# Kernel optimization log

Hardware: AMD Instinct MI355X
Metric: run time of the kernel (lower is better)

The kernel has to match this reference:

```python
import jax, jax.numpy as jnp
import numpy as np

HIDDEN = 2048
NUM_HEADS = 16
HEAD_DIM = HIDDEN // NUM_HEADS


def setup_inputs() -> dict:
    key = jax.random.key(0)
    k1, k2, k3 = jax.random.split(key, 3)
    hidden_states = jax.random.normal(k1, (4, 2048, HIDDEN), dtype=jnp.float32)
    # torch Linear weight is (out, in); y = x @ W.T. Store transposed (in, out).
    w_qkv = jax.random.normal(k2, (HIDDEN, 3 * HIDDEN), dtype=jnp.float32) * (HIDDEN ** -0.5)
    w_o = jax.random.normal(k3, (HIDDEN, HIDDEN), dtype=jnp.float32) * (HIDDEN ** -0.5)
    return {"hidden_states": hidden_states, "w_qkv": w_qkv, "w_o": w_o}


def reference(hidden_states, w_qkv, w_o):
    B, S, _ = hidden_states.shape
    qkv = hidden_states @ w_qkv  # (B, S, 3*HIDDEN)
    # Faithful to torch .view: row-major reshape straight to (B, H, S, 3*head_dim)
    qkv = qkv.reshape(B, NUM_HEADS, S, 3 * HEAD_DIM)
    q, k, v = jnp.split(qkv, 3, axis=-1)  # each (B, H, S, head_dim)
    scores = jnp.einsum('bhsd,bhtd->bhst', q, k) / (HEAD_DIM ** 0.5)
    probs = jax.nn.softmax(scores, axis=-1)
    attn = jnp.einsum('bhst,bhtd->bhsd', probs, v)  # (B, H, S, head_dim)
    # Faithful to torch .reshape(B, S, hidden) without transpose
    attn = attn.reshape(B, S, HIDDEN)
    return attn @ w_o
```

## Files before the change

### kernel.cpp

```cpp
#include <hip/hip_runtime.h>
#include <stdint.h>

#define DEVINL __device__ __forceinline__

typedef __attribute__((ext_vector_type(8))) __bf16 bf16x8;
typedef __attribute__((ext_vector_type(4))) float f32x4;
typedef __attribute__((ext_vector_type(16))) float f32x16;

static constexpr int HID  = 2048;
static constexpr int NQ   = 6144;
static constexpr int SEQ  = 2048;
static constexpr int NB   = 4;
static constexpr int MTOT = NB * SEQ;

DEVINL unsigned short f2bf(float f) {
  union { float f; uint32_t u; } x; x.f = f;
  uint32_t r = x.u + 0x7fffu + ((x.u >> 16) & 1u);
  return (unsigned short)(r >> 16);
}

DEVINL float fexp2(float x) { float r; asm("v_exp_f32 %0, %1" : "=v"(r) : "v"(x)); return r; }

typedef const __attribute__((address_space(1))) void gvoid_t;
typedef __attribute__((address_space(3))) void svoid_t;

DEVINL void gload_lds16(const void* g, void* s) {
  __builtin_amdgcn_global_load_lds((gvoid_t*)(uintptr_t)g,
                                   (svoid_t*)(uint32_t)(uintptr_t)s,
                                   16, 0, 0);
}


__global__ void k_cvt(const float* __restrict__ in, unsigned short* __restrict__ out, int n4) {
  int i = blockIdx.x * blockDim.x + threadIdx.x;
  if (i >= n4) return;
  float4 v = ((const float4*)in)[i];
  ushort4 o;
  o.x = f2bf(v.x); o.y = f2bf(v.y); o.z = f2bf(v.z); o.w = f2bf(v.w);
  ((ushort4*)out)[i] = o;
}

__global__ void k_transpose_cvt(const float* __restrict__ in, unsigned short* __restrict__ out,
                                int R, int C) {
  __shared__ float tile[32][33];
  int c0 = blockIdx.x * 32, r0 = blockIdx.y * 32;
  int tx = threadIdx.x & 31, ty = threadIdx.x >> 5;
  #pragma unroll
  for (int i = 0; i < 32; i += 8)
    tile[ty + i][tx] = in[(size_t)(r0 + ty + i) * C + (c0 + tx)];
  __syncthreads();
  #pragma unroll
  for (int i = 0; i < 32; i += 8)
    out[(size_t)(c0 + ty + i) * R + (r0 + tx)] = f2bf(tile[tx][ty + i]);
}


template <int OUT_BF16, int QSCALE>
__global__ __launch_bounds__(256, 2) void k_gemm2(const unsigned short* __restrict__ A,
                                                  const unsigned short* __restrict__ BT,
                                                  void* __restrict__ Cout,
                                                  int M, int N, int K) {
  __shared__ unsigned short As[256 * 64];
  __shared__ unsigned short Bs[128 * 64];
  const int tid = threadIdx.x;
  const int w = tid >> 6, l = tid & 63;
  const int lane16 = l & 15, lgrp = l >> 4;
  const int bn = blockIdx.x, bm = blockIdx.y;
  const int srow = l >> 3;
  const int gslot = (l & 7) ^ (l >> 3);

  f32x4 acc[4][8] = {};

  for (int k0 = 0; k0 < K; k0 += 64) {
    #pragma unroll
    for (int i = 0; i < 8; ++i) {
      const int chunk = i * 4 + w;
      const int row = chunk * 8 + srow;
      gload_lds16(A + (size_t)(bm * 256 + row) * K + k0 + gslot * 8, As + chunk * 512);
    }
    #pragma unroll
    for (int i = 0; i < 4; ++i) {
      const int chunk = i * 4 + w;
      const int row = chunk * 8 + srow;
      gload_lds16(BT + (size_t)(bn * 128 + row) * K + k0 + gslot * 8, Bs + chunk * 512);
    }
    __syncthreads();

    #pragma unroll
    for (int kk = 0; kk < 2; ++kk) {
      bf16x8 af[4], bfr[8];
      #pragma unroll
      for (int mf = 0; mf < 4; ++mf) {
        const int row = w * 64 + mf * 16 + lane16;
        af[mf] = *(const bf16x8*)(As + row * 64 + (((kk * 4 + lgrp) ^ (row & 7)) * 8));
      }
      #pragma unroll
      for (int nf = 0; nf < 8; ++nf) {
        const int row = nf * 16 + lane16;
        bfr[nf] = *(const bf16x8*)(Bs + row * 64 + (((kk * 4 + lgrp) ^ (row & 7)) * 8));
      }
      #pragma unroll
      for (int mf = 0; mf < 4; ++mf)
        #pragma unroll
        for (int nf = 0; nf < 8; ++nf)
          acc[mf][nf] = __builtin_amdgcn_mfma_f32_16x16x32_bf16(af[mf], bfr[nf], acc[mf][nf], 0, 0, 0);
    }
    __syncthreads();
  }

  const float qs = (QSCALE && (bn % 3 == 0)) ? 0.12751744f : 1.0f;
  const size_t row0 = (size_t)bm * 256 + w * 64;
  const int col0 = bn * 128;
  #pragma unroll
  for (int mf = 0; mf < 4; ++mf) {
    #pragma unroll
    for (int nf = 0; nf < 8; ++nf) {
      const int col = col0 + nf * 16 + lane16;
      #pragma unroll
      for (int r = 0; r < 4; ++r) {
        const size_t row = row0 + mf * 16 + lgrp * 4 + r;
        if (OUT_BF16)
          ((unsigned short*)Cout)[row * N + col] = f2bf(acc[mf][nf][r] * qs);
        else
          ((float*)Cout)[row * N + col] = acc[mf][nf][r];
      }
    }
  }
}

__global__ __launch_bounds__(256, 2) void k_build_vt2(const unsigned short* __restrict__ QKV,
                                                      unsigned short* __restrict__ Vt) {
  __shared__ unsigned short lt[128][136];
  const int head = blockIdx.y;
  const int tblk = blockIdx.x;
  const int b = head >> 4, h = head & 15;
  const int base_row = b * SEQ + h * 128;
  const int tid = threadIdx.x;

  #pragma unroll
  for (int it = 0; it < 8; ++it) {
    const int idx = it * 256 + tid;
    const int tt = idx >> 4, dgrp = idx & 15;
    const uint4 v = *(const uint4*)(QKV + (size_t)(base_row + tblk * 8 + (tt >> 4)) * NQ
                                        + (tt & 15) * 384 + 256 + dgrp * 8);
    *(uint4*)(&lt[tt][dgrp * 8]) = v;
  }
  __syncthreads();

  #pragma unroll
  for (int it = 0; it < 8; ++it) {
    const int idx = it * 256 + tid;
    const int d = idx >> 4, tgrp = idx & 15;
    ushort4 a, bq;
    a.x = lt[tgrp * 8 + 0][d]; a.y = lt[tgrp * 8 + 1][d];
    a.z = lt[tgrp * 8 + 2][d]; a.w = lt[tgrp * 8 + 3][d];
    bq.x = lt[tgrp * 8 + 4][d]; bq.y = lt[tgrp * 8 + 5][d];
    bq.z = lt[tgrp * 8 + 6][d]; bq.w = lt[tgrp * 8 + 7][d];
    unsigned short* dst = Vt + ((size_t)head * 128 + d) * SEQ + tblk * 128 + tgrp * 8;
    *(ushort4*)(dst) = a;
    *(ushort4*)(dst + 4) = bq;
  }
}

__global__ __launch_bounds__(256, 2) void k_attn(const unsigned short* __restrict__ QKV,
                                                 const unsigned short* __restrict__ Vt,
                                                 unsigned short* __restrict__ ATT) {
  __shared__ unsigned short Ks[2][64 * 128];
  __shared__ unsigned short Vs[128 * 64];
  const int tid = threadIdx.x, w = tid >> 6, l = tid & 63;
  const int l32 = l & 31, hi = l >> 5;
  const int qt = blockIdx.x, head = blockIdx.y;
  const int b = head >> 4, h = head & 15;
  const float THR = 11.5415603f;
  const int base_row = b * SEQ + h * 128;

  const int s = qt * 128 + w * 32 + l32;
  bf16x8 qf[8];
  {
    const unsigned short* qrow = QKV + (size_t)(base_row + (s >> 4)) * NQ + (s & 15) * 384;
    #pragma unroll
    for (int dsl = 0; dsl < 8; ++dsl)
      qf[dsl] = *(const bf16x8*)(qrow + dsl * 16 + hi * 8);
  }

  f32x16 oacc[4] = {};
  float mrun = -1e30f, lrun = 0.0f;

  #define STAGE_K(bb, kv0)                                                               \
    {                                                                                    \
      _Pragma("unroll")                                                                  \
      for (int i = 0; i < 4; ++i) {                                                      \
        const int chunk = i * 4 + w;                                                     \
        const int r = chunk * 4 + (l >> 4);                                              \
        const int colsw = ((l & 15) ^ (r & 15)) * 8;                                     \
        gload_lds16(QKV + (size_t)(base_row + ((kv0) >> 4) + (r >> 4)) * NQ              \
                        + (r & 15) * 384 + 128 + colsw,                                  \
                    &Ks[bb][chunk * 512]);                                               \
      }                                                                                  \
    }
  #define STAGE_V(kv0)                                                                   \
    {                                                                                    \
      _Pragma("unroll")                                                                  \
      for (int i = 0; i < 4; ++i) {                                                      \
        const int chunk = i * 4 + w;                                                     \
        const int dr = chunk * 8 + (l >> 3);                                             \
        const int colsw = ((l & 7) ^ (dr & 7)) * 8;                                      \
        gload_lds16(Vt + ((size_t)head * 128 + dr) * SEQ + (kv0) + colsw,                \
                    &Vs[chunk * 512]);                                                   \
      }                                                                                  \
    }

  STAGE_K(0, 0);
  STAGE_V(0);
  __syncthreads();

  int kb = 0;
  for (int kv0 = 0; kv0 < SEQ; kv0 += 64) {
    const int next = kv0 + 64;
    if (next < SEQ) STAGE_K(kb ^ 1, next);

    f32x16 sacc[2] = {};
    __builtin_amdgcn_s_setprio(1);
    #pragma unroll
    for (int kvf = 0; kvf < 2; ++kvf) {
      const int row = kvf * 32 + l32;
      const unsigned short* kbase = &Ks[kb][row * 128];
      const int rs = (row & 15) << 3;
      #pragma unroll
      for (int dsl = 0; dsl < 8; ++dsl) {
        bf16x8 kf = *(const bf16x8*)(kbase + ((dsl * 16 + hi * 8) ^ rs));
        sacc[kvf] = __builtin_amdgcn_mfma_f32_32x32x16_bf16(kf, qf[dsl], sacc[kvf], 0, 0, 0);
      }
    }
    __builtin_amdgcn_s_setprio(0);

    float mx[16];
    #pragma unroll
    for (int r = 0; r < 16; ++r) mx[r] = fmaxf(sacc[0][r], sacc[1][r]);
    #pragma unroll
    for (int st = 8; st >= 1; st >>= 1)
      #pragma unroll
      for (int r = 0; r < st; ++r) mx[r] = fmaxf(mx[r], mx[r + st]);
    float pmax = fmaxf(mx[0], __shfl_xor(mx[0], 32));

    if (!__all(pmax - mrun <= THR)) {
      const float mnew = fmaxf(mrun, pmax);
      const float corr = fexp2(mrun - mnew);
      #pragma unroll
      for (int df = 0; df < 4; ++df)
        #pragma unroll
        for (int r = 0; r < 16; ++r) oacc[df][r] *= corr;
      lrun *= corr;
      mrun = mnew;
    }

    float ps[16];
    #pragma unroll
    for (int r = 0; r < 16; ++r) {
      const float p0 = fexp2(sacc[0][r] - mrun);
      const float p1 = fexp2(sacc[1][r] - mrun);
      sacc[0][r] = p0; sacc[1][r] = p1;
      ps[r] = p0 + p1;
    }
    #pragma unroll
    for (int st = 8; st >= 1; st >>= 1)
      #pragma unroll
      for (int r = 0; r < st; ++r) ps[r] += ps[r + st];
    lrun += ps[0] + __shfl_xor(ps[0], 32);

    bf16x8 pf[4];
    #pragma unroll
    for (int f = 0; f < 2; ++f) {
      unsigned int c0, c1, c2, c3, c4, c5, c6, c7;
      asm("v_cvt_pk_bf16_f32 %0, %1, %2" : "=v"(c0) : "v"(sacc[f][0]),  "v"(sacc[f][1]));
      asm("v_cvt_pk_bf16_f32 %0, %1, %2" : "=v"(c1) : "v"(sacc[f][2]),  "v"(sacc[f][3]));
      asm("v_cvt_pk_bf16_f32 %0, %1, %2" : "=v"(c2) : "v"(sacc[f][4]),  "v"(sacc[f][5]));
      asm("v_cvt_pk_bf16_f32 %0, %1, %2" : "=v"(c3) : "v"(sacc[f][6]),  "v"(sacc[f][7]));
      asm("v_cvt_pk_bf16_f32 %0, %1, %2" : "=v"(c4) : "v"(sacc[f][8]),  "v"(sacc[f][9]));
      asm("v_cvt_pk_bf16_f32 %0, %1, %2" : "=v"(c5) : "v"(sacc[f][10]), "v"(sacc[f][11]));
      asm("v_cvt_pk_bf16_f32 %0, %1, %2" : "=v"(c6) : "v"(sacc[f][12]), "v"(sacc[f][13]));
      asm("v_cvt_pk_bf16_f32 %0, %1, %2" : "=v"(c7) : "v"(sacc[f][14]), "v"(sacc[f][15]));
      asm("v_permlane32_swap_b32 %0, %1" : "+v"(c0), "+v"(c2));
      asm("v_permlane32_swap_b32 %0, %1" : "+v"(c1), "+v"(c3));
      asm("v_permlane32_swap_b32 %0, %1" : "+v"(c4), "+v"(c6));
      asm("v_permlane32_swap_b32 %0, %1" : "+v"(c5), "+v"(c7));
      union { unsigned int u[4]; bf16x8 v; } u0, u1;
      u0.u[0] = c0; u0.u[1] = c1; u0.u[2] = c2; u0.u[3] = c3;
      u1.u[0] = c4; u1.u[1] = c5; u1.u[2] = c6; u1.u[3] = c7;
      pf[2 * f] = u0.v; pf[2 * f + 1] = u1.v;
    }

    __syncthreads();

    __builtin_amdgcn_s_setprio(1);
    #pragma unroll
    for (int ks = 0; ks < 4; ++ks) {
      #pragma unroll
      for (int df = 0; df < 4; ++df) {
        const int row = df * 32 + l32;
        bf16x8 vf = *(const bf16x8*)(&Vs[row * 64 + (((ks * 16 + hi * 8) ^ ((row & 7) << 3)))]);
        oacc[df] = __builtin_amdgcn_mfma_f32_32x32x16_bf16(vf, pf[ks], oacc[df], 0, 0, 0);
      }
    }
    __builtin_amdgcn_s_setprio(0);

    __syncthreads();
    if (next < SEQ) STAGE_V(next);
    kb ^= 1;
  }

  const float inv = 1.0f / lrun;
  unsigned short* orow = ATT + (size_t)(base_row + (s >> 4)) * HID + (s & 15) * 128;
  #pragma unroll
  for (int df = 0; df < 4; ++df) {
    #pragma unroll
    for (int k = 0; k < 4; ++k) {
      ushort4 o;
      o.x = f2bf(oacc[df][4 * k + 0] * inv);
      o.y = f2bf(oacc[df][4 * k + 1] * inv);
      o.z = f2bf(oacc[df][4 * k + 2] * inv);
      o.w = f2bf(oacc[df][4 * k + 3] * inv);
      *(ushort4*)(orow + df * 32 + 8 * k + 4 * hi) = o;
    }
  }
}


extern "C" void kernel_launch(void* const* d_in, const int* in_sizes, int n_in,
                              void* d_out, int out_size, void* d_ws, size_t ws_size,
                              hipStream_t stream) {
  const float* X    = (const float*)d_in[0];
  const float* Wqkv = (const float*)d_in[1];
  const float* Wo   = (const float*)d_in[2];
  float* OUT = (float*)d_out;

  char* ws = (char*)d_ws;
  constexpr size_t SZ_QKV   = (size_t)MTOT * NQ * 2;
  constexpr size_t SZ_XBF   = (size_t)MTOT * HID * 2;
  constexpr size_t SZ_WQKVT = (size_t)NQ * HID * 2;
  constexpr size_t SZ_WOT   = (size_t)HID * HID * 2;
  constexpr size_t SZ_VT    = (size_t)64 * 128 * SEQ * 2;
  unsigned short* QKV   = (unsigned short*)(ws);
  unsigned short* Xbf   = (unsigned short*)(ws + SZ_QKV);
  unsigned short* WqkvT = (unsigned short*)(ws + SZ_QKV + SZ_XBF);
  unsigned short* WoT   = (unsigned short*)(ws + SZ_QKV + SZ_XBF + SZ_WQKVT);
  unsigned short* Vt    = (unsigned short*)(ws + SZ_QKV + SZ_XBF + SZ_WQKVT + SZ_WOT);
  unsigned short* ATT   = (unsigned short*)(ws + SZ_QKV + SZ_XBF + SZ_WQKVT + SZ_WOT + SZ_VT);

  k_cvt<<<(MTOT * HID / 4 + 255) / 256, 256, 0, stream>>>(X, Xbf, MTOT * HID / 4);
  k_transpose_cvt<<<dim3(NQ / 32, HID / 32), 256, 0, stream>>>(Wqkv, WqkvT, HID, NQ);
  k_transpose_cvt<<<dim3(HID / 32, HID / 32), 256, 0, stream>>>(Wo, WoT, HID, HID);
  k_gemm2<1, 1><<<dim3(NQ / 128, MTOT / 256), 256, 0, stream>>>(Xbf, WqkvT, QKV, MTOT, NQ, HID);
  k_build_vt2<<<dim3(16, 64), 256, 0, stream>>>(QKV, Vt);
  k_attn<<<dim3(16, 64), 256, 0, stream>>>(QKV, Vt, ATT);
  k_gemm2<0, 0><<<dim3(HID / 128, MTOT / 256), 256, 0, stream>>>(ATT, WoT, OUT, MTOT, HID, HID);
}
```

Baseline: 461.0 us.

## Fuse prep conversions into one kernel and double attention query tile per block

Merges the X conversion and the two weight transpose-conversions into a single launch, dispatched by block index, which removes two kernel launches. The attention kernel now uses 512 threads (8 waves) over 256 query rows per block, so each staged K/V tile in LDS is shared by twice as many queries and K/V global traffic is halved. The risk is that the 512-thread blocks with launch_bounds(512,4) may limit occupancy or registers, and half as many attention blocks are launched. Any code in the unseen parts that still assumes 4 waves would break this change.

```diff
diff --git a/kernel.cpp b/kernel.cpp
--- a/kernel.cpp
+++ b/kernel.cpp
@@ -30,21 +30,34 @@
                                    16, 0, 0);
 }
 
-
-__global__ void k_cvt(const float* __restrict__ in, unsigned short* __restrict__ out, int n4) {
-  int i = blockIdx.x * blockDim.x + threadIdx.x;
-  if (i >= n4) return;
-  float4 v = ((const float4*)in)[i];
-  ushort4 o;
-  o.x = f2bf(v.x); o.y = f2bf(v.y); o.z = f2bf(v.z); o.w = f2bf(v.w);
-  ((ushort4*)out)[i] = o;
-}
-
-__global__ void k_transpose_cvt(const float* __restrict__ in, unsigned short* __restrict__ out,
-                                int R, int C) {
+__global__ __launch_bounds__(256, 2) void k_prep(const float* __restrict__ X,
+                                                 const float* __restrict__ Wqkv,
+                                                 const float* __restrict__ Wo,
+                                                 unsigned short* __restrict__ Xbf,
+                                                 unsigned short* __restrict__ WqkvT,
+                                                 unsigned short* __restrict__ WoT) {
   __shared__ float tile[32][33];
-  int c0 = blockIdx.x * 32, r0 = blockIdx.y * 32;
-  int tx = threadIdx.x & 31, ty = threadIdx.x >> 5;
+  const int bid = blockIdx.x;
+  if (bid < 16384) {
+    const int i = bid * 256 + threadIdx.x;
+    float4 v = ((const float4*)X)[i];
+    ushort4 o;
+    o.x = f2bf(v.x); o.y = f2bf(v.y); o.z = f2bf(v.z); o.w = f2bf(v.w);
+    ((ushort4*)Xbf)[i] = o;
+    return;
+  }
+  const float* in; unsigned short* out; int R, C, bx, by;
+  if (bid < 16384 + 12288) {
+    const int r = bid - 16384;
+    in = Wqkv; out = WqkvT; R = HID; C = NQ;
+    bx = r % (NQ / 32); by = r / (NQ / 32);
+  } else {
+    const int r = bid - 16384 - 12288;
+    in = Wo; out = WoT; R = HID; C = HID;
+    bx = r % (HID / 32); by = r / (HID / 32);
+  }
+  const int c0 = bx * 32, r0 = by * 32;
+  const int tx = threadIdx.x & 31, ty = threadIdx.x >> 5;
   #pragma unroll
   for (int i = 0; i < 32; i += 8)
     tile[ty + i][tx] = in[(size_t)(r0 + ty + i) * C + (c0 + tx)];
@@ -162,7 +175,7 @@
   }
 }
 
-__global__ __launch_bounds__(256, 2) void k_attn(const unsigned short* __restrict__ QKV,
+__global__ __launch_bounds__(512, 4) void k_attn(const unsigned short* __restrict__ QKV,
                                                  const unsigned short* __restrict__ Vt,
                                                  unsigned short* __restrict__ ATT) {
   __shared__ unsigned short Ks[2][64 * 128];
@@ -174,7 +187,7 @@
   const float THR = 11.5415603f;
   const int base_row = b * SEQ + h * 128;
 
-  const int s = qt * 128 + w * 32 + l32;
+  const int s = qt * 256 + w * 32 + l32;
   bf16x8 qf[8];
   {
     const unsigned short* qrow = QKV + (size_t)(base_row + (s >> 4)) * NQ + (s & 15) * 384;
@@ -189,8 +202,8 @@
   #define STAGE_K(bb, kv0)                                                               \
     {                                                                                    \
       _Pragma("unroll")                                                                  \
-      for (int i = 0; i < 4; ++i) {                                                      \
-        const int chunk = i * 4 + w;                                                     \
+      for (int i = 0; i < 2; ++i) {                                                      \
+        const int chunk = i * 8 + w;                                                     \
         const int r = chunk * 4 + (l >> 4);                                              \
         const int colsw = ((l & 15) ^ (r & 15)) * 8;                                     \
         gload_lds16(QKV + (size_t)(base_row + ((kv0) >> 4) + (r >> 4)) * NQ              \
@@ -201,8 +214,8 @@
   #define STAGE_V(kv0)                                                                   \
     {                                                                                    \
       _Pragma("unroll")                                                                  \
-      for (int i = 0; i < 4; ++i) {                                                      \
-        const int chunk = i * 4 + w;                                                     \
+      for (int i = 0; i < 2; ++i) {                                                      \
+        const int chunk = i * 8 + w;                                                     \
         const int dr = chunk * 8 + (l >> 3);                                             \
         const int colsw = ((l & 7) ^ (dr & 7)) * 8;                                      \
         gload_lds16(Vt + ((size_t)head * 128 + dr) * SEQ + (kv0) + colsw,                \
@@ -347,11 +360,9 @@
   unsigned short* Vt    = (unsigned short*)(ws + SZ_QKV + SZ_XBF + SZ_WQKVT + SZ_WOT);
   unsigned short* ATT   = (unsigned short*)(ws + SZ_QKV + SZ_XBF + SZ_WQKVT + SZ_WOT + SZ_VT);
 
-  k_cvt<<<(MTOT * HID / 4 + 255) / 256, 256, 0, stream>>>(X, Xbf, MTOT * HID / 4);
-  k_transpose_cvt<<<dim3(NQ / 32, HID / 32), 256, 0, stream>>>(Wqkv, WqkvT, HID, NQ);
-  k_transpose_cvt<<<dim3(HID / 32, HID / 32), 256, 0, stream>>>(Wo, WoT, HID, HID);
+  k_prep<<<16384 + 12288 + 4096, 256, 0, stream>>>(X, Wqkv, Wo, Xbf, WqkvT, WoT);
   k_gemm2<1, 1><<<dim3(NQ / 128, MTOT / 256), 256, 0, stream>>>(Xbf, WqkvT, QKV, MTOT, NQ, HID);
   k_build_vt2<<<dim3(16, 64), 256, 0, stream>>>(QKV, Vt);
-  k_attn<<<dim3(16, 64), 256, 0, stream>>>(QKV, Vt, ATT);
+  k_attn<<<dim3(8, 64), 512, 0, stream>>>(QKV, Vt, ATT);
   k_gemm2<0, 0><<<dim3(HID / 128, MTOT / 256), 256, 0, stream>>>(ATT, WoT, OUT, MTOT, HID, HID);
 }
```

New measurement: 799.2 us. +73.4%, slower.
